# Performance work log

Hardware: AMD Instinct MI355X
Metric: run time of the kernel (lower is better)

## Reference

```python
import jax, jax.numpy as jnp
import numpy as np

GROUP = 8
BS = 4096
CH = 512


def setup_inputs() -> dict:
    key = jax.random.key(0)
    k1, k2 = jax.random.split(key)
    x = jax.random.normal(k1, (GROUP, BS, CH), dtype=jnp.float32)
    stdv = 1.0 / np.sqrt(CH)  # reset_parameters: uniform(-stdv, stdv), stdv = 1/sqrt(channels)
    weight = jax.random.uniform(k2, (GROUP, CH, CH), minval=-stdv, maxval=stdv, dtype=jnp.float32)
    return {"x": x, "weight": weight}


def reference(x, weight):
    """Sequential per-channel Householder reflections.

    x: (group, bs, channels); weight: (group, channels, channels).
    Step i uses v_i = weight[:, :, i] and applies
        x <- x - 2/(v^T v) * (x @ v) v^T
    """
    vs = jnp.transpose(weight, (2, 0, 1))  # (channels, group, channels): scan axis first

    def step(x, v):
        denom = jnp.sum(v * v, axis=-1)          # (group,)   v^T v
        proj = jnp.einsum('gbc,gc->gb', x, v)    # (group, bs) x @ v
        x = x - (2.0 / denom)[:, None, None] * proj[:, :, None] * v[:, None, :]
        return x, None

    x, _ = jax.lax.scan(step, x, vs)
    return x
```

## Files before the change

kernel.cpp:

```cpp
#include <hip/hip_runtime.h>

#define GROUP 8
#define BS 4096
#define CH 512
#define PW 32
#define NPANEL 16

typedef __attribute__((ext_vector_type(4))) float f32x4;
typedef __attribute__((ext_vector_type(8))) short bf16x8;
typedef __attribute__((ext_vector_type(8))) unsigned short u16x8;
typedef unsigned short u16;

static __device__ __forceinline__ u16 f2bf(float f) {
    unsigned int u = __builtin_bit_cast(unsigned int, f);
    u += 0x7FFFu + ((u >> 16) & 1u);
    return (u16)(u >> 16);
}
static __device__ __forceinline__ float bf2f(u16 h) {
    return __builtin_bit_cast(float, (unsigned int)h << 16);
}
static __device__ __forceinline__ void split8(const float* v, bf16x8& h, bf16x8& l) {
#pragma unroll
    for (int j = 0; j < 8; ++j) {
        u16 hu = f2bf(v[j]);
        h[j] = (short)hu;
        l[j] = (short)f2bf(v[j] - bf2f(hu));
    }
}
#define MFMA(a, b, c) __builtin_amdgcn_mfma_f32_16x16x32_bf16(a, b, c, 0, 0, 0)

typedef const __attribute__((address_space(1))) void* gas_t;
typedef __attribute__((address_space(3))) void* las_t;
static __device__ __forceinline__ void gload16(const void* g, void* l) {
    __builtin_amdgcn_global_load_lds((gas_t)g, (las_t)l, 16, 0, 0);
}


__global__ __launch_bounds__(1024) void k_panelprep(const float* __restrict__ w,
                                                    const float* __restrict__ x,
                                                    u16* __restrict__ Yfh,
                                                    u16* __restrict__ Yfl,
                                                    u16* __restrict__ Mfh,
                                                    u16* __restrict__ Mfl,
                                                    u16* __restrict__ Afh,
                                                    u16* __restrict__ Afl,
                                                    u16* __restrict__ xb) {
    __shared__ float Ylds[PW][516];
    __shared__ float Sp[16][PW][36];
    __shared__ float S_ls[PW][36];
    __shared__ float T_ls[PW][36];

    int bid = blockIdx.x;
    int t   = threadIdx.x;

    if (bid >= 128) {
        const int TOT8 = GROUP * BS * CH / 8;
        for (int i = (bid - 128) * 1024 + t; i < TOT8; i += 1024 * 1024) {
            const float4* s = (const float4*)(x + (size_t)i * 8);
            float4 a = s[0], b = s[1];
            u16x8 o;
            o[0] = f2bf(a.x); o[1] = f2bf(a.y); o[2] = f2bf(a.z); o[3] = f2bf(a.w);
            o[4] = f2bf(b.x); o[5] = f2bf(b.y); o[6] = f2bf(b.z); o[7] = f2bf(b.w);
            *(u16x8*)(xb + (size_t)i * 8) = o;
        }
        return;
    }

    int pb   = (bid & 7) * 16 + (bid >> 3);
    int lane = t & 63;
    int wv   = t >> 6;
    int fr   = lane & 15;
    int kg   = lane >> 4;
    int g    = pb >> 4;
    int p    = pb & 15;
    int i0   = p * PW;

    const float* wg = w + (size_t)g * CH * CH;
    for (int idx4 = t; idx4 < 4096; idx4 += 1024) {
        int c = idx4 >> 3, f4 = idx4 & 7;
        float4 v = *(const float4*)(wg + (size_t)c * CH + i0 + f4 * 4);
        Ylds[f4 * 4 + 0][c] = v.x;
        Ylds[f4 * 4 + 1][c] = v.y;
        Ylds[f4 * 4 + 2][c] = v.z;
        Ylds[f4 * 4 + 3][c] = v.w;
    }
    __syncthreads();

    {
        f32x4 sacc[2][2];
#pragma unroll
        for (int a = 0; a < 2; ++a)
#pragma unroll
            for (int b = 0; b < 2; ++b)
#pragma unroll
                for (int z = 0; z < 4; ++z) sacc[a][b][z] = 0.f;
        {
            int kk = wv;
            bf16x8 fh[2], fl[2];
#pragma unroll
            for (int h = 0; h < 2; ++h) {
                float a8[8];
                const float* src = &Ylds[h * 16 + fr][kk * 32 + kg * 8];
#pragma unroll
                for (int j = 0; j < 8; ++j) a8[j] = src[j];
                split8(a8, fh[h], fl[h]);
            }
#pragma unroll
            for (int a = 0; a < 2; ++a)
#pragma unroll
                for (int b = 0; b < 2; ++b) {
                    sacc[a][b] = MFMA(fh[a], fh[b], sacc[a][b]);
                    sacc[a][b] = MFMA(fh[a], fl[b], sacc[a][b]);
                    sacc[a][b] = MFMA(fl[a], fh[b], sacc[a][b]);
                }
        }
#pragma unroll
        for (int a = 0; a < 2; ++a)
#pragma unroll
            for (int b = 0; b < 2; ++b)
#pragma unroll
                for (int j = 0; j < 4; ++j)
                    Sp[wv][a * 16 + kg * 4 + j][b * 16 + fr] = sacc[a][b][j];
    }
    __syncthreads();
    for (int idx = t; idx < PW * PW; idx += 1024) {
        int r = idx >> 5, c = idx & 31;
        float s = 0.f;
#pragma unroll
        for (int q = 0; q < 16; ++q) s += Sp[q][r][c];
        S_ls[r][c] = s;
    }
    __syncthreads();

    if (wv == 0) {
        float Trow[PW];
#pragma unroll
        for (int j = 0; j < PW; ++j) Trow[j] = 0.f;
        if (lane < PW) Trow[lane] = 2.0f / S_ls[lane][lane];
#pragma unroll
        for (int k = 1; k < PW; ++k) {
            float acc = 0.f;
#pragma unroll
            for (int j = 0; j < PW; ++j)
                if (j < k) acc += Trow[j] * S_ls[j][k];
            float bk = 2.0f / S_ls[k][k];
            if (lane < k) Trow[k] = -bk * acc;
        }
        if (lane < PW)
#pragma unroll
            for (int j = 0; j < PW; ++j) T_ls[lane][j] = Trow[j];
    }
    __syncthreads();

    u16* Msth = (u16*)Sp;
    u16* Mstl = Msth + 16384;
    {
        bf16x8 tbh[2], tbl[2];
#pragma unroll
        for (int cf = 0; cf < 2; ++cf) {
            float t8[8];
            const float* src = &T_ls[cf * 16 + fr][kg * 8];
#pragma unroll
            for (int j = 0; j < 8; ++j) t8[j] = src[j];
            split8(t8, tbh[cf], tbl[cf]);
        }
#pragma unroll
        for (int rfi = 0; rfi < 2; ++rfi) {
            int rf = 2 * wv + rfi;
            float a8[8];
#pragma unroll
            for (int j = 0; j < 8; ++j) a8[j] = Ylds[kg * 8 + j][rf * 16 + fr];
            bf16x8 ah, al;
            split8(a8, ah, al);
#pragma unroll
            for (int cf = 0; cf < 2; ++cf) {
                f32x4 m;
#pragma unroll
                for (int z = 0; z < 4; ++z) m[z] = 0.f;
                m = MFMA(ah, tbh[cf], m);
                m = MFMA(ah, tbl[cf], m);
                m = MFMA(al, tbh[cf], m);
#pragma unroll
                for (int j = 0; j < 4; ++j) {
                    int c  = rf * 16 + kg * 4 + j;
                    int ii = cf * 16 + fr;
                    int off = ((c >> 4)) * 512 + ((ii >> 3) * 16 + (c & 15)) * 8 + (ii & 7);
                    u16 hu = f2bf(m[j]);
                    Msth[off] = hu;
                    Mstl[off] = f2bf(m[j] - bf2f(hu));
                }
            }
        }
    }
    __syncthreads();
    {
        u16* Mfh_g = Mfh + (size_t)g * CH * CH + (size_t)p * 16384;
        u16* Mfl_g = Mfl + (size_t)g * CH * CH + (size_t)p * 16384;
        for (int idx = t; idx < 2048; idx += 1024) {
            *(bf16x8*)(Mfh_g + (size_t)idx * 8) = *(const bf16x8*)(Msth + idx * 8);
            *(bf16x8*)(Mfl_g + (size_t)idx * 8) = *(const bf16x8*)(Mstl + idx * 8);
        }
    }

    {
        u16* Yfh_g = Yfh + (size_t)g * CH * CH;
        u16* Yfl_g = Yfl + (size_t)g * CH * CH;
        for (int idx = t; idx < 32 * 64; idx += 1024) {
            int tile = idx >> 6, l2 = idx & 63;
            int itl = tile >> 4, ct = tile & 15;
            int row = l2 & 15, kgg = l2 >> 4;
            float a8[8];
            const float* src = &Ylds[itl * 16 + row][ct * 32 + kgg * 8];
#pragma unroll
            for (int j = 0; j < 8; ++j) a8[j] = src[j];
            bf16x8 h, l;
            split8(a8, h, l);
            size_t off = ((size_t)((2 * p + itl) * 16 + ct)) * 512 + (size_t)l2 * 8;
            *(bf16x8*)(Yfh_g + off) = h;
            *(bf16x8*)(Yfl_g + off) = l;
        }
    }

    {
        u16* Afh_g = Afh + (size_t)g * CH * CH;
        u16* Afl_g = Afl + (size_t)g * CH * CH;
        for (int idx = t; idx < 32 * 64; idx += 1024) {
            int mt = idx >> 6, l2 = idx & 63;
            int row = l2 & 15, kg2 = l2 >> 4;
            float a8[8];
#pragma unroll
            for (int j = 0; j < 8; ++j) a8[j] = Ylds[kg2 * 8 + j][mt * 16 + row];
            bf16x8 h, l;
            split8(a8, h, l);
            size_t off = ((size_t)(p * 32 + mt)) * 512 + (size_t)l2 * 8;
            *(bf16x8*)(Afh_g + off) = h;
            *(bf16x8*)(Afl_g + off) = l;
        }
    }
}

template<int W>
__global__ __launch_bounds__(512) void k_combine(const u16* __restrict__ Yfh,
                                                 const u16* __restrict__ Yfl,
                                                 u16* __restrict__ Mfh,
                                                 u16* __restrict__ Mfl) {
    constexpr int NF   = W / 16;
    constexpr int KSPL = (NF >= 8) ? 1 : 8 / NF;
    constexpr int CPW  = (NF + 7) / 8;

    __shared__ u16 MAh[16][520];
    __shared__ u16 MAl[16][520];
    __shared__ float Cl[16][W + 4];
    __shared__ float Cpart[(KSPL > 1) ? (KSPL - 1) : 1][16][W + 4];

    int bid = blockIdx.x;
    int cb  = (bid & 7) * 16 + (bid >> 3);
    int t = threadIdx.x, lane = t & 63, wv = t >> 6;
    int fr = lane & 15, kg = lane >> 4;
    int g  = cb >> 4;
    int sg = cb & 15;
    constexpr int SP = W / 16;
    int q  = sg / SP, rs = sg % SP;
    int i_top0 = 2 * q * W + rs * 16;
    int i_bot0 = 2 * q * W + W;

    const u16* Yfh_g = Yfh + (size_t)g * CH * CH;
    const u16* Yfl_g = Yfl + (size_t)g * CH * CH;
    u16* Mfh_g = Mfh + (size_t)g * CH * CH;
    u16* Mfl_g = Mfl + (size_t)g * CH * CH;

    int kt_top = i_top0 >> 5;
    int hh     = (i_top0 & 31) >> 3;

    for (int idx = t; idx < 1024; idx += 512) {
        int c = idx >> 1, sub = idx & 1;
        size_t off = ((size_t)(kt_top * 32 + (c >> 4))) * 512
                   + (size_t)((hh + sub) * 16 + (c & 15)) * 8;
        bf16x8 hv = *(const bf16x8*)(Mfh_g + off);
        bf16x8 lv = *(const bf16x8*)(Mfl_g + off);
#pragma unroll
        for (int j = 0; j < 8; ++j) {
            MAh[sub * 8 + j][c] = (u16)hv[j];
            MAl[sub * 8 + j][c] = (u16)lv[j];
        }
    }
    __syncthreads();

    int ibt = i_bot0 >> 4;

    if constexpr (KSPL == 1) {
        f32x4 accC[CPW];
#pragma unroll
        for (int nfi = 0; nfi < CPW; ++nfi)
#pragma unroll
            for (int z = 0; z < 4; ++z) accC[nfi][z] = 0.f;

        for (int ks = 0; ks < 16; ++ks) {
            bf16x8 ah = *(const bf16x8*)&MAh[fr][ks * 32 + kg * 8];
            bf16x8 al = *(const bf16x8*)&MAl[fr][ks * 32 + kg * 8];
#pragma unroll
            for (int nfi = 0; nfi < CPW; ++nfi) {
                int nf = wv + 8 * nfi;
                if (nf < NF) {
                    size_t yo = ((size_t)((ibt + nf) * 16 + ks)) * 512 + (size_t)lane * 8;
                    bf16x8 bh = *(const bf16x8*)(Yfh_g + yo);
                    bf16x8 bl = *(const bf16x8*)(Yfl_g + yo);
                    accC[nfi] = MFMA(ah, bh, accC[nfi]);
                    accC[nfi] = MFMA(ah, bl, accC[nfi]);
                    accC[nfi] = MFMA(al, bh, accC[nfi]);
                }
            }
        }
#pragma unroll
        for (int nfi = 0; nfi < CPW; ++nfi) {
            int nf = wv + 8 * nfi;
            if (nf < NF)
#pragma unroll
                for (int jj = 0; jj < 4; ++jj)
                    Cl[kg * 4 + jj][nf * 16 + fr] = accC[nfi][jj];
        }
        __syncthreads();
    } else {
        int nf  = wv % NF;
        int ksl = wv / NF;
        constexpr int KCH = 16 / KSPL;
        f32x4 accC;
#pragma unroll
        for (int z = 0; z < 4; ++z) accC[z] = 0.f;

        for (int ki = 0; ki < KCH; ++ki) {
            int ks = ksl * KCH + ki;
            bf16x8 ah = *(const bf16x8*)&MAh[fr][ks * 32 + kg * 8];
            bf16x8 al = *(const bf16x8*)&MAl[fr][ks * 32 + kg * 8];
            size_t yo = ((size_t)((ibt + nf) * 16 + ks)) * 512 + (size_t)lane * 8;
            bf16x8 bh = *(const bf16x8*)(Yfh_g + yo);
            bf16x8 bl = *(const bf16x8*)(Yfl_g + yo);
            accC = MFMA(ah, bh, accC);
            accC = MFMA(ah, bl, accC);
            accC = MFMA(al, bh, accC);
        }
        if (ksl == 0) {
#pragma unroll
            for (int jj = 0; jj < 4; ++jj)
                Cl[kg * 4 + jj][nf * 16 + fr] = accC[jj];
        } else {
#pragma unroll
            for (int jj = 0; jj < 4; ++jj)
                Cpart[ksl - 1][kg * 4 + jj][nf * 16 + fr] = accC[jj];
        }
        __syncthreads();
        for (int idx = t; idx < 16 * W; idx += 512) {
            int r = idx / W, c = idx - r * W;
            float s = Cl[r][c];
#pragma unroll
            for (int u = 0; u < KSPL - 1; ++u) s += Cpart[u][r][c];
            Cl[r][c] = s;
        }
        __syncthreads();
    }

    f32x4 accU[4];
#pragma unroll
    for (int ni = 0; ni < 4; ++ni)
#pragma unroll
        for (int z = 0; z < 4; ++z) accU[ni][z] = 0.f;

    int kt_bot = i_bot0 >> 5;
    for (int ks2 = 0; ks2 < W / 32; ++ks2) {
        float a8[8];
#pragma unroll
        for (int j = 0; j < 8; ++j) a8[j] = Cl[fr][ks2 * 32 + kg * 8 + j];
        bf16x8 ah2, al2;
        split8(a8, ah2, al2);
#pragma unroll
        for (int ni = 0; ni < 4; ++ni) {
            int ct = wv * 4 + ni;
            size_t mo = ((size_t)((kt_bot + ks2) * 32 + ct)) * 512 + (size_t)lane * 8;
            bf16x8 bh = *(const bf16x8*)(Mfh_g + mo);
            bf16x8 bl = *(const bf16x8*)(Mfl_g + mo);
            accU[ni] = MFMA(ah2, bh, accU[ni]);
            accU[ni] = MFMA(ah2, bl, accU[ni]);
            accU[ni] = MFMA(al2, bh, accU[ni]);
        }
    }
#pragma unroll
    for (int ni = 0; ni < 4; ++ni) {
        int c = (wv * 4 + ni) * 16 + fr;
#pragma unroll
        for (int jj = 0; jj < 4; ++jj) {
            int il = kg * 4 + jj;
            float ma = bf2f(MAh[il][c]) + bf2f(MAl[il][c]);
            float m2 = ma - accU[ni][jj];
            u16 hu = f2bf(m2);
            MAh[il][c] = hu;
            MAl[il][c] = f2bf(m2 - bf2f(hu));
        }
    }
    __syncthreads();

    for (int idx = t; idx < 1024; idx += 512) {
        int c = idx >> 1, sub = idx & 1;
        bf16x8 hv, lv;
#pragma unroll
        for (int j = 0; j < 8; ++j) {
            hv[j] = (short)MAh[sub * 8 + j][c];
            lv[j] = (short)MAl[sub * 8 + j][c];
        }
        size_t off = ((size_t)(kt_top * 32 + (c >> 4))) * 512
                   + (size_t)((hh + sub) * 16 + (c & 15)) * 8;
        *(bf16x8*)(Mfh_g + off) = hv;
        *(bf16x8*)(Mfl_g + off) = lv;
    }
}

__global__ __launch_bounds__(256) void k_qbuild2(const u16* __restrict__ Afh,
                                                 const u16* __restrict__ Afl,
                                                 const u16* __restrict__ Mfh,
                                                 const u16* __restrict__ Mfl,
                                                 u16* __restrict__ Qt) {
    int bid = blockIdx.x;
    int qb  = (bid & 7) * 64 + (bid >> 3);
    int t = threadIdx.x, lane = t & 63, wv = t >> 6;
    int fr = lane & 15, kg = lane >> 4;
    int g  = qb >> 6;
    int tm = (qb >> 2) & 15, tn = qb & 3;
    int c0 = tm * 32;
    int d0 = tn * 128 + wv * 32;

    const u16* Afh_g = Afh + (size_t)g * CH * CH;
    const u16* Afl_g = Afl + (size_t)g * CH * CH;
    const u16* Mfh_g = Mfh + (size_t)g * CH * CH;
    const u16* Mfl_g = Mfl + (size_t)g * CH * CH;
    u16* Qt_g = Qt + (size_t)g * CH * CH;

    f32x4 acc[2][2];
#pragma unroll
    for (int mi = 0; mi < 2; ++mi)
#pragma unroll
        for (int ni = 0; ni < 2; ++ni)
#pragma unroll
            for (int z = 0; z < 4; ++z) acc[mi][ni][z] = 0.f;

    int mt0 = c0 >> 4;
    for (int ks = 0; ks < 16; ++ks) {
        bf16x8 ah[2], al[2], bh[2], bl[2];
#pragma unroll
        for (int mi = 0; mi < 2; ++mi) {
            size_t ao = ((size_t)(ks * 32 + mt0 + mi)) * 512 + (size_t)lane * 8;
            ah[mi] = *(const bf16x8*)(Afh_g + ao);
            al[mi] = *(const bf16x8*)(Afl_g + ao);
        }
#pragma unroll
        for (int ni = 0; ni < 2; ++ni) {
            int ct = (d0 >> 4) + ni;
            size_t mo = ((size_t)(ks * 32 + ct)) * 512 + (size_t)lane * 8;
            bh[ni] = *(const bf16x8*)(Mfh_g + mo);
            bl[ni] = *(const bf16x8*)(Mfl_g + mo);
        }
#pragma unroll
        for (int mi = 0; mi < 2; ++mi)
#pragma unroll
            for (int ni = 0; ni < 2; ++ni) {
                acc[mi][ni] = MFMA(ah[mi], bh[ni], acc[mi][ni]);
                acc[mi][ni] = MFMA(ah[mi], bl[ni], acc[mi][ni]);
                acc[mi][ni] = MFMA(al[mi], bh[ni], acc[mi][ni]);
            }
    }
#pragma unroll
    for (int mi = 0; mi < 2; ++mi)
#pragma unroll
        for (int ni = 0; ni < 2; ++ni) {
            int cb2 = c0 + mi * 16 + kg * 4;
            int d   = d0 + ni * 16 + fr;
            ushort4 h4;
            h4.x = f2bf(((cb2 + 0 == d) ? 1.0f : 0.0f) - acc[mi][ni][0]);
            h4.y = f2bf(((cb2 + 1 == d) ? 1.0f : 0.0f) - acc[mi][ni][1]);
            h4.z = f2bf(((cb2 + 2 == d) ? 1.0f : 0.0f) - acc[mi][ni][2]);
            h4.w = f2bf(((cb2 + 3 == d) ? 1.0f : 0.0f) - acc[mi][ni][3]);
            *(ushort4*)(Qt_g + (size_t)d * CH + cb2) = h4;
        }
}

__global__ __launch_bounds__(256) void k_gemm2(const u16* __restrict__ xb,
                                               const u16* __restrict__ Qt,
                                               float* __restrict__ out) {
    __shared__ u16 Ab[2][128 * 32];
    __shared__ u16 Bb[2][128 * 32];

    int bid0 = blockIdx.x;
    int wg = (bid0 & 7) * 128 + (bid0 >> 3);
    int g  = wg >> 7;
    int r  = wg & 127;
    int tm = r >> 2;
    int tn = r & 3;

    int t    = threadIdx.x;
    int lane = t & 63;
    int wv   = t >> 6;
    int wr   = wv >> 1, wc = wv & 1;
    int fr   = lane & 15, kg = lane >> 4;

    const u16* xg  = xb + (size_t)g * BS * CH + (size_t)tm * 128 * CH;
    const u16* Qtg = Qt + (size_t)g * CH * CH + (size_t)tn * 128 * CH;
    float* og = out + (size_t)g * BS * CH + (size_t)tm * 128 * CH + (size_t)tn * 128;

    f32x4 acc[4][4];
#pragma unroll
    for (int mi = 0; mi < 4; ++mi)
#pragma unroll
        for (int ni = 0; ni < 4; ++ni)
#pragma unroll
            for (int z = 0; z < 4; ++z) acc[mi][ni][z] = 0.f;

    int srow = lane >> 2;
    int scol = (lane & 3) * 8;

    auto STAGE = [&](int p, int ks) {
        int k0 = ks * 32;
#pragma unroll
        for (int si = 0; si < 2; ++si) {
            int seg = wv * 2 + si;
            int row = seg * 16 + srow;
            gload16(xg  + (size_t)row * CH + k0 + scol, &Ab[p][seg * 512]);
            gload16(Qtg + (size_t)row * CH + k0 + scol, &Bb[p][seg * 512]);
        }
    };

    STAGE(0, 0);
    asm volatile("s_waitcnt vmcnt(0)" ::: "memory");
    __builtin_amdgcn_s_barrier();

    for (int ks = 0; ks < 16; ++ks) {
        int cur = ks & 1;
        if (ks < 15) {
            STAGE(cur ^ 1, ks + 1);
            asm volatile("s_waitcnt vmcnt(4)" ::: "memory");
        } else {
            asm volatile("s_waitcnt vmcnt(0)" ::: "memory");
        }
        __builtin_amdgcn_s_barrier();

        bf16x8 af[4], bfr[4];
#pragma unroll
        for (int mi = 0; mi < 4; ++mi)
            af[mi] = *(const bf16x8*)&Ab[cur][(wr * 64 + mi * 16 + fr) * 32 + kg * 8];
#pragma unroll
        for (int ni = 0; ni < 4; ++ni)
            bfr[ni] = *(const bf16x8*)&Bb[cur][(wc * 64 + ni * 16 + fr) * 32 + kg * 8];
#pragma unroll
        for (int mi = 0; mi < 4; ++mi)
#pragma unroll
            for (int ni = 0; ni < 4; ++ni)
                acc[mi][ni] = MFMA(af[mi], bfr[ni], acc[mi][ni]);

        asm volatile("" ::: "memory");
        __builtin_amdgcn_s_barrier();
    }

    int rg = lane >> 4;
#pragma unroll
    for (int mi = 0; mi < 4; ++mi)
#pragma unroll
        for (int ni = 0; ni < 4; ++ni)
#pragma unroll
            for (int rj = 0; rj < 4; ++rj) {
                int grow = wr * 64 + mi * 16 + rg * 4 + rj;
                int gcol = wc * 64 + ni * 16 + fr;
                og[(size_t)grow * CH + gcol] = acc[mi][ni][rj];
            }
}

#define LDP 40
__global__ __launch_bounds__(256) void k_gemm_f32(const float* __restrict__ x,
                                                  const u16* __restrict__ Qt,
                                                  float* __restrict__ out) {
    __shared__ u16 Al[128 * LDP];
    __shared__ u16 Bl[128 * LDP];

    int bid = blockIdx.x;
    int g  = bid >> 7;
    int tn = (bid >> 5) & 3;
    int tm = bid & 31;

    int t    = threadIdx.x;
    int lane = t & 63;
    int w    = t >> 6;
    int wr   = w >> 1, wc = w & 1;

    const float* xg = x + (size_t)g * BS * CH + (size_t)tm * 128 * CH;
    const u16* Qtg = Qt + (size_t)g * CH * CH + (size_t)tn * 128 * CH;
    float* og = out + (size_t)g * BS * CH + (size_t)tm * 128 * CH + (size_t)tn * 128;

    f32x4 acc[4][4];
#pragma unroll
    for (int mi = 0; mi < 4; ++mi)
#pragma unroll
        for (int ni = 0; ni < 4; ++ni)
#pragma unroll
            for (int z = 0; z < 4; ++z) acc[mi][ni][z] = 0.f;

    int a_k4 = t & 7;
    int a_r  = t >> 3;
    int b_n  = t & 127;
    int b_kh = t >> 7;
    int fr = lane & 15, kg = lane >> 4;

    for (int ks = 0; ks < 16; ++ks) {
        int k0 = ks * 32;
        __syncthreads();
#pragma unroll
        for (int rr = 0; rr < 4; ++rr) {
            int r = a_r + 32 * rr;
            float4 v = *(const float4*)(xg + (size_t)r * CH + k0 + a_k4 * 4);
            ushort4 h;
            h.x = f2bf(v.x); h.y = f2bf(v.y); h.z = f2bf(v.z); h.w = f2bf(v.w);
            *(ushort4*)(&Al[r * LDP + a_k4 * 4]) = h;
        }
        {
            const u16* src = Qtg + (size_t)b_n * CH + k0 + b_kh * 16;
            u16x8 lo = *(const u16x8*)src;
            u16x8 hi = *(const u16x8*)(src + 8);
            *(u16x8*)(&Bl[b_n * LDP + b_kh * 16]) = lo;
            *(u16x8*)(&Bl[b_n * LDP + b_kh * 16 + 8]) = hi;
        }
        __syncthreads();
        bf16x8 af[4], bfr[4];
#pragma unroll
        for (int mi = 0; mi < 4; ++mi)
            af[mi] = *(const bf16x8*)(&Al[(wr * 64 + mi * 16 + fr) * LDP + kg * 8]);
#pragma unroll
        for (int ni = 0; ni < 4; ++ni)
            bfr[ni] = *(const bf16x8*)(&Bl[(wc * 64 + ni * 16 + fr) * LDP + kg * 8]);
#pragma unroll
        for (int mi = 0; mi < 4; ++mi)
#pragma unroll
            for (int ni = 0; ni < 4; ++ni)
                acc[mi][ni] = MFMA(af[mi], bfr[ni], acc[mi][ni]);
    }

    int rg = lane >> 4;
#pragma unroll
    for (int mi = 0; mi < 4; ++mi)
#pragma unroll
        for (int ni = 0; ni < 4; ++ni)
#pragma unroll
            for (int rj = 0; rj < 4; ++rj) {
                int grow = wr * 64 + mi * 16 + rg * 4 + rj;
                int gcol = wc * 64 + ni * 16 + fr;
                og[(size_t)grow * CH + gcol] = acc[mi][ni][rj];
            }
}

extern "C" void kernel_launch(void* const* d_in, const int* in_sizes, int n_in,
                              void* d_out, int out_size, void* d_ws, size_t ws_size,
                              hipStream_t stream) {
    const float* x = (const float*)d_in[0];
    const float* w = (const float*)d_in[1];
    float* out = (float*)d_out;

    char* ob = (char*)d_out;
    u16* Yfh = (u16*)ob;
    u16* Yfl = (u16*)(ob + (4u  << 20));
    u16* Mfh = (u16*)(ob + (8u  << 20));
    u16* Mfl = (u16*)(ob + (12u << 20));
    u16* Afh = (u16*)(ob + (16u << 20));
    u16* Afl = (u16*)(ob + (20u << 20));

    int fat = (ws_size >= ((32u << 20) + (4u << 20))) ? 1 : 0;
    u16* xbp = (u16*)d_ws;
    u16* Qt  = fat ? (u16*)((char*)d_ws + (32u << 20)) : (u16*)d_ws;

    k_panelprep<<<dim3(fat ? 1152 : 128), dim3(1024), 0, stream>>>(w, x, Yfh, Yfl, Mfh, Mfl, Afh, Afl, xbp);
    k_combine<32><<<dim3(128), dim3(512), 0, stream>>>(Yfh, Yfl, Mfh, Mfl);
    k_combine<64><<<dim3(128), dim3(512), 0, stream>>>(Yfh, Yfl, Mfh, Mfl);
    k_combine<128><<<dim3(128), dim3(512), 0, stream>>>(Yfh, Yfl, Mfh, Mfl);
    k_combine<256><<<dim3(128), dim3(512), 0, stream>>>(Yfh, Yfl, Mfh, Mfl);
    k_qbuild2<<<dim3(512), dim3(256), 0, stream>>>(Afh, Afl, Mfh, Mfl, Qt);
    if (fat)
        k_gemm2<<<dim3(1024), dim3(256), 0, stream>>>(xbp, Qt, out);
    else
        k_gemm_f32<<<dim3(1024), dim3(256), 0, stream>>>(x, Qt, out);
}
```

Baseline: 106.0 us.

## Software-prefetch global MFMA operands, remap x-conversion blocks per XCD, add setprio

The panel-update loops now load the next k-step's Y and M fragments from global memory into registers while the current step's MFMAs run, so memory latency overlaps with compute. The x-to-bf16 conversion blocks are remapped so each XCD converts one contiguous group slice, presumably for cache locality, and each block handles a fixed 2048 units instead of a grid-stride loop. The main GEMM raises wave priority around its MFMA burst. The nf<NF guard is dropped in the KSPL==1 path, which assumes CPW*8 equals NF, and double-buffered registers raise register pressure.

```diff
diff --git a/kernel.cpp b/kernel.cpp
--- a/kernel.cpp
+++ b/kernel.cpp
@@ -54,8 +54,13 @@
     int t   = threadIdx.x;
 
     if (bid >= 128) {
-        const int TOT8 = GROUP * BS * CH / 8;
-        for (int i = (bid - 128) * 1024 + t; i < TOT8; i += 1024 * 1024) {
+        int bx  = bid - 128;
+        int xcd = bx & 7;
+        int j   = bx >> 3;
+        const int UPG = (BS * CH) / 8;
+        int base = xcd * UPG + j * (UPG / 128);
+        for (int u = t; u < 2048; u += 1024) {
+            int i = base + u;
             const float4* s = (const float4*)(x + (size_t)i * 8);
             float4 a = s[0], b = s[1];
             u16x8 o;
@@ -295,29 +300,39 @@
 #pragma unroll
             for (int z = 0; z < 4; ++z) accC[nfi][z] = 0.f;
 
+        auto LOADY = [&](int ks, bf16x8* dh, bf16x8* dl) {
+#pragma unroll
+            for (int nfi = 0; nfi < CPW; ++nfi) {
+                int nf = wv + 8 * nfi;
+                size_t yo = ((size_t)((ibt + nf) * 16 + ks)) * 512 + (size_t)lane * 8;
+                dh[nfi] = *(const bf16x8*)(Yfh_g + yo);
+                dl[nfi] = *(const bf16x8*)(Yfl_g + yo);
+            }
+        };
+
+        bf16x8 pbh[CPW], pbl[CPW];
+        LOADY(0, pbh, pbl);
+#pragma unroll
         for (int ks = 0; ks < 16; ++ks) {
+            bf16x8 qbh[CPW], qbl[CPW];
+            if (ks + 1 < 16) LOADY(ks + 1, qbh, qbl);
             bf16x8 ah = *(const bf16x8*)&MAh[fr][ks * 32 + kg * 8];
             bf16x8 al = *(const bf16x8*)&MAl[fr][ks * 32 + kg * 8];
 #pragma unroll
             for (int nfi = 0; nfi < CPW; ++nfi) {
-                int nf = wv + 8 * nfi;
-                if (nf < NF) {
-                    size_t yo = ((size_t)((ibt + nf) * 16 + ks)) * 512 + (size_t)lane * 8;
-                    bf16x8 bh = *(const bf16x8*)(Yfh_g + yo);
-                    bf16x8 bl = *(const bf16x8*)(Yfl_g + yo);
-                    accC[nfi] = MFMA(ah, bh, accC[nfi]);
-                    accC[nfi] = MFMA(ah, bl, accC[nfi]);
-                    accC[nfi] = MFMA(al, bh, accC[nfi]);
-                }
+                accC[nfi] = MFMA(ah, pbh[nfi], accC[nfi]);
+                accC[nfi] = MFMA(ah, pbl[nfi], accC[nfi]);
+                accC[nfi] = MFMA(al, pbh[nfi], accC[nfi]);
             }
+#pragma unroll
+            for (int nfi = 0; nfi < CPW; ++nfi) { pbh[nfi] = qbh[nfi]; pbl[nfi] = qbl[nfi]; }
         }
 #pragma unroll
         for (int nfi = 0; nfi < CPW; ++nfi) {
             int nf = wv + 8 * nfi;
-            if (nf < NF)
-#pragma unroll
-                for (int jj = 0; jj < 4; ++jj)
-                    Cl[kg * 4 + jj][nf * 16 + fr] = accC[nfi][jj];
+#pragma unroll
+            for (int jj = 0; jj < 4; ++jj)
+                Cl[kg * 4 + jj][nf * 16 + fr] = accC[nfi][jj];
         }
         __syncthreads();
     } else {
@@ -328,16 +343,25 @@
 #pragma unroll
         for (int z = 0; z < 4; ++z) accC[z] = 0.f;
 
+        auto LOADY1 = [&](int ks, bf16x8& dh, bf16x8& dl) {
+            size_t yo = ((size_t)((ibt + nf) * 16 + ks)) * 512 + (size_t)lane * 8;
+            dh = *(const bf16x8*)(Yfh_g + yo);
+            dl = *(const bf16x8*)(Yfl_g + yo);
+        };
+
+        bf16x8 pbh, pbl;
+        LOADY1(ksl * KCH, pbh, pbl);
+#pragma unroll
         for (int ki = 0; ki < KCH; ++ki) {
             int ks = ksl * KCH + ki;
+            bf16x8 qbh, qbl;
+            if (ki + 1 < KCH) LOADY1(ks + 1, qbh, qbl);
             bf16x8 ah = *(const bf16x8*)&MAh[fr][ks * 32 + kg * 8];
             bf16x8 al = *(const bf16x8*)&MAl[fr][ks * 32 + kg * 8];
-            size_t yo = ((size_t)((ibt + nf) * 16 + ks)) * 512 + (size_t)lane * 8;
-            bf16x8 bh = *(const bf16x8*)(Yfh_g + yo);
-            bf16x8 bl = *(const bf16x8*)(Yfl_g + yo);
-            accC = MFMA(ah, bh, accC);
-            accC = MFMA(ah, bl, accC);
-            accC = MFMA(al, bh, accC);
+            accC = MFMA(ah, pbh, accC);
+            accC = MFMA(ah, pbl, accC);
+            accC = MFMA(al, pbh, accC);
+            pbh = qbh; pbl = qbl;
         }
         if (ksl == 0) {
 #pragma unroll
@@ -366,21 +390,38 @@
         for (int z = 0; z < 4; ++z) accU[ni][z] = 0.f;
 
     int kt_bot = i_bot0 >> 5;
-    for (int ks2 = 0; ks2 < W / 32; ++ks2) {
-        float a8[8];
-#pragma unroll
-        for (int j = 0; j < 8; ++j) a8[j] = Cl[fr][ks2 * 32 + kg * 8 + j];
-        bf16x8 ah2, al2;
-        split8(a8, ah2, al2);
+    constexpr int NKS2 = W / 32;
+
+    auto LOADM = [&](int ks2, bf16x8* dh, bf16x8* dl) {
 #pragma unroll
         for (int ni = 0; ni < 4; ++ni) {
             int ct = wv * 4 + ni;
             size_t mo = ((size_t)((kt_bot + ks2) * 32 + ct)) * 512 + (size_t)lane * 8;
-            bf16x8 bh = *(const bf16x8*)(Mfh_g + mo);
-            bf16x8 bl = *(const bf16x8*)(Mfl_g + mo);
-            accU[ni] = MFMA(ah2, bh, accU[ni]);
-            accU[ni] = MFMA(ah2, bl, accU[ni]);
-            accU[ni] = MFMA(al2, bh, accU[ni]);
+            dh[ni] = *(const bf16x8*)(Mfh_g + mo);
+            dl[ni] = *(const bf16x8*)(Mfl_g + mo);
+        }
+    };
+
+    {
+        bf16x8 mph[4], mpl[4];
+        LOADM(0, mph, mpl);
+#pragma unroll
+        for (int ks2 = 0; ks2 < NKS2; ++ks2) {
+            bf16x8 mqh[4], mql[4];
+            if (ks2 + 1 < NKS2) LOADM(ks2 + 1, mqh, mql);
+            float a8[8];
+#pragma unroll
+            for (int j = 0; j < 8; ++j) a8[j] = Cl[fr][ks2 * 32 + kg * 8 + j];
+            bf16x8 ah2, al2;
+            split8(a8, ah2, al2);
+#pragma unroll
+            for (int ni = 0; ni < 4; ++ni) {
+                accU[ni] = MFMA(ah2, mph[ni], accU[ni]);
+                accU[ni] = MFMA(ah2, mpl[ni], accU[ni]);
+                accU[ni] = MFMA(al2, mph[ni], accU[ni]);
+            }
+#pragma unroll
+            for (int ni = 0; ni < 4; ++ni) { mph[ni] = mqh[ni]; mpl[ni] = mql[ni]; }
         }
     }
 #pragma unroll
@@ -547,11 +588,13 @@
 #pragma unroll
         for (int ni = 0; ni < 4; ++ni)
             bfr[ni] = *(const bf16x8*)&Bb[cur][(wc * 64 + ni * 16 + fr) * 32 + kg * 8];
+        __builtin_amdgcn_s_setprio(1);
 #pragma unroll
         for (int mi = 0; mi < 4; ++mi)
 #pragma unroll
             for (int ni = 0; ni < 4; ++ni)
                 acc[mi][ni] = MFMA(af[mi], bfr[ni], acc[mi][ni]);
+        __builtin_amdgcn_s_setprio(0);
 
         asm volatile("" ::: "memory");
         __builtin_amdgcn_s_barrier();
```

Result: faster. 102.0 us (-3.7%).
